# Performance work log

Measured on AMD Instinct MI355X. Metric: run time of the kernel, lower is better.

Reference implementation:

```python
import jax, jax.numpy as jnp
import numpy as np

EPS = 1e-5

def setup_inputs() -> dict:
    key = jax.random.key(0)
    k1, k2 = jax.random.split(key)
    x = jax.random.normal(k1, (16, 512, 128, 128), dtype=jnp.float32)
    classifier_w = jax.random.normal(k2, (19, 512), dtype=jnp.float32)
    sel = jnp.arange(16, dtype=jnp.int32)  # selected_classes
    return {"x": x, "classifier_w": classifier_w, "sel": sel}


def reference(x, classifier_w, sel):
    # x: [B, ch, H, W]; classifier_w: [num_classes, ch]; sel: [C] class ids
    B, ch, H, W = x.shape
    C = sel.shape[0]
    G = ch // C            # number of channel groups
    HW = H * W

    w_abs = jnp.abs(classifier_w)          # [K, ch]
    idx = jnp.argsort(-w_abs, axis=1)      # descending sort indices [K, ch]
    sig = jax.nn.sigmoid(w_abs)            # [K, ch]

    idx_sel = idx[sel]                     # [C, ch]
    ch_ids = idx_sel[:, :G].T              # [G, C]; ch_ids[k, j] = idx[sel[j]][k]
    perm = ch_ids.reshape(G * C)           # output channel C*k+j <- input channel
    wgh = sig[sel[None, :], ch_ids].reshape(G * C)  # sigmoid weights per output channel

    # fused gather + scale (replaces the triple Python loop)
    xs = x[:, perm] * wgh[None, :, None, None]      # [B, G*C, H, W]
    xg = xs.reshape(B, G, C, HW)                    # groups of C channels

    # per-group covariance: bmm(x, x^T) / (HW - 1) + eps*I
    cov = jnp.einsum('bgch,bgdh->bgcd', xg, xg) / (HW - 1)
    cov = cov + EPS * jnp.eye(C, dtype=x.dtype)

    mask = jnp.triu(jnp.ones((C, C), dtype=x.dtype), k=1)  # reversal_i
    num_off = jnp.sum(mask)                # C*(C-1)/2 off-diagonal entries

    # relax_denom == 0 -> margin = 0
    off = jnp.sum(jnp.abs(cov * mask), axis=(2, 3))         # [B, G]
    loss_per = jnp.maximum(off / num_off, 0.0)              # clamp(min=0)
    loss = jnp.sum(loss_per) / B           # per-group mean over B, summed over groups
    return loss.reshape(1)
```

## Files before the change

### kernel.cpp

```cpp
#include <hip/hip_runtime.h>
#include <math.h>

constexpr int B_  = 16;
constexpr int CH  = 512;
constexpr int HW  = 128 * 128;
constexpr int C_  = 16;
constexpr int G_  = 32;
constexpr int NP  = (C_ * (C_ - 1)) / 2;

__global__ __launch_bounds__(64)
void topk_kernel(const float* __restrict__ w, const int* __restrict__ sel,
                 int* __restrict__ perm_tbl, float* __restrict__ wgh_tbl) {
  const int j    = blockIdx.x;
  const int lane = threadIdx.x;
  const float* wr = w + (size_t)sel[j] * CH;

  float vals[8];
#pragma unroll
  for (int i = 0; i < 8; ++i) vals[i] = fabsf(wr[lane * 8 + i]);

  for (int k = 0; k < G_; ++k) {
    float bv = vals[0];
    int bloc = 0;
#pragma unroll
    for (int i = 1; i < 8; ++i)
      if (vals[i] > bv) { bv = vals[i]; bloc = i; }
    int bi = lane * 8 + bloc;

#pragma unroll
    for (int m = 1; m < 64; m <<= 1) {
      float ov = __shfl_xor(bv, m);
      int   oi = __shfl_xor(bi, m);
      if (ov > bv || (ov == bv && oi < bi)) { bv = ov; bi = oi; }
    }

    if (lane == 0) {
      perm_tbl[k * C_ + j] = bi;
      wgh_tbl [k * C_ + j] = 1.0f / (1.0f + expf(-bv));
    }

    if ((bi >> 3) == lane) {
#pragma unroll
      for (int i = 0; i < 8; ++i)
        if ((bi & 7) == i) vals[i] = -1.0f;
    }
  }
}

__global__ __launch_bounds__(256, 2)
void gram_kernel(const float* __restrict__ x, const int* __restrict__ perm_tbl,
                 const float* __restrict__ wgh_tbl, float* __restrict__ out) {
  const int bg = blockIdx.x;
  const int b  = bg >> 5;
  const int g  = bg & (G_ - 1);
  const int t  = threadIdx.x;

  __shared__ int   s_ch[C_];
  __shared__ float s_w[C_];
  if (t < C_) {
    s_ch[t] = perm_tbl[g * C_ + t];
    s_w[t]  = wgh_tbl[g * C_ + t];
  }
  __syncthreads();

  const float* bb = x + (size_t)b * ((size_t)CH * HW);
  int off[C_];
#pragma unroll
  for (int c = 0; c < C_; ++c) off[c] = s_ch[c] * HW;

  float acc[NP];
#pragma unroll
  for (int i = 0; i < NP; ++i) acc[i] = 0.0f;

  for (int it = 0; it < HW / (256 * 2); ++it) {
    const int h = (it * 256 + t) * 2;
    float2 v[C_];
#pragma unroll
    for (int c = 0; c < C_; ++c)
      v[c] = *(const float2*)(bb + off[c] + h);

    int p = 0;
#pragma unroll
    for (int c = 0; c < C_; ++c) {
#pragma unroll
      for (int d = c + 1; d < C_; ++d) {
        acc[p] = fmaf(v[c].x, v[d].x, acc[p]);
        acc[p] = fmaf(v[c].y, v[d].y, acc[p]);
        ++p;
      }
    }
  }

  const int lane = t & 63;
  const int wv   = t >> 6;
#pragma unroll
  for (int i = 0; i < NP; ++i) {
    float a = acc[i];
#pragma unroll
    for (int m = 1; m < 64; m <<= 1) a += __shfl_xor(a, m);
    acc[i] = a;
  }

  __shared__ float s_part[4][NP];
  if (lane == 0) {
#pragma unroll
    for (int i = 0; i < NP; ++i) s_part[wv][i] = acc[i];
  }
  __syncthreads();

  __shared__ float s_fin[128];
  if (t < 128) {
    float s = 0.0f;
    if (t < NP) {
      s = s_part[0][t] + s_part[1][t] + s_part[2][t] + s_part[3][t];
      int cc = 0, rem = t;
      while (rem >= (C_ - 1) - cc) { rem -= (C_ - 1) - cc; ++cc; }
      int dd = cc + 1 + rem;
      s = fabsf(s) * s_w[cc] * s_w[dd];
    }
    s_fin[t] = s;
  }
  __syncthreads();

  for (int st = 64; st > 0; st >>= 1) {
    if (t < st) s_fin[t] += s_fin[t + st];
    __syncthreads();
  }

  if (t == 0) {
    constexpr float SCALE = 1.0f / (120.0f * 16383.0f * 16.0f);
    atomicAdd(out, s_fin[0] * SCALE);
  }
}

extern "C" void kernel_launch(void* const* d_in, const int* in_sizes, int n_in,
                              void* d_out, int out_size, void* d_ws, size_t ws_size,
                              hipStream_t stream) {
  const float* x   = (const float*)d_in[0];
  const float* w   = (const float*)d_in[1];
  const int*   sel = (const int*)d_in[2];
  float*       out = (float*)d_out;

  int*   perm_tbl = (int*)d_ws;
  float* wgh_tbl  = (float*)((char*)d_ws + CH * sizeof(int));

  hipMemsetAsync(d_out, 0, sizeof(float), stream);

  hipLaunchKernelGGL(topk_kernel, dim3(C_), dim3(64), 0, stream,
                     w, sel, perm_tbl, wgh_tbl);
  hipLaunchKernelGGL(gram_kernel, dim3(B_ * G_), dim3(256), 0, stream,
                     x, perm_tbl, wgh_tbl, out);
}
```

Baseline: 687.6 us.

## Split Gram reduction over spatial chunks with a separate finalize kernel

The spatial dimension is split into four chunks, so the Gram kernel launches four times as many blocks. Each block writes partial pair sums to workspace, and a new finalize kernel combines them, applies abs and the sigmoid weights, and does the atomic add. With only 512 blocks on a large GPU the original grid left compute units underused for a bandwidth-bound read of 512MB. The change adds a third kernel launch and a small round trip of partial sums through global memory.

```diff
diff --git a/kernel.cpp b/kernel.cpp
--- a/kernel.cpp
+++ b/kernel.cpp
@@ -7,6 +7,8 @@
 constexpr int C_  = 16;
 constexpr int G_  = 32;
 constexpr int NP  = (C_ * (C_ - 1)) / 2;
+constexpr int NSPLIT = 4;
+constexpr int HWS = HW / NSPLIT;
 
 __global__ __launch_bounds__(64)
 void topk_kernel(const float* __restrict__ w, const int* __restrict__ sel,
@@ -48,22 +50,21 @@
 }
 
 __global__ __launch_bounds__(256, 2)
-void gram_kernel(const float* __restrict__ x, const int* __restrict__ perm_tbl,
-                 const float* __restrict__ wgh_tbl, float* __restrict__ out) {
-  const int bg = blockIdx.x;
-  const int b  = bg >> 5;
-  const int g  = bg & (G_ - 1);
-  const int t  = threadIdx.x;
+void gram_part_kernel(const float* __restrict__ x,
+                      const int* __restrict__ perm_tbl,
+                      float* __restrict__ part) {
+  const int bid   = blockIdx.x;
+  const int split = bid & (NSPLIT - 1);
+  const int bg    = bid >> 2;
+  const int b     = bg >> 5;
+  const int g     = bg & (G_ - 1);
+  const int t     = threadIdx.x;
 
-  __shared__ int   s_ch[C_];
-  __shared__ float s_w[C_];
-  if (t < C_) {
-    s_ch[t] = perm_tbl[g * C_ + t];
-    s_w[t]  = wgh_tbl[g * C_ + t];
-  }
+  __shared__ int s_ch[C_];
+  if (t < C_) s_ch[t] = perm_tbl[g * C_ + t];
   __syncthreads();
 
-  const float* bb = x + (size_t)b * ((size_t)CH * HW);
+  const float* bb = x + (size_t)b * ((size_t)CH * HW) + split * HWS;
   int off[C_];
 #pragma unroll
   for (int c = 0; c < C_; ++c) off[c] = s_ch[c] * HW;
@@ -72,7 +73,7 @@
 #pragma unroll
   for (int i = 0; i < NP; ++i) acc[i] = 0.0f;
 
-  for (int it = 0; it < HW / (256 * 2); ++it) {
+  for (int it = 0; it < HWS / (256 * 2); ++it) {
     const int h = (it * 256 + t) * 2;
     float2 v[C_];
 #pragma unroll
@@ -108,28 +109,41 @@
   }
   __syncthreads();
 
-  __shared__ float s_fin[128];
-  if (t < 128) {
-    float s = 0.0f;
-    if (t < NP) {
-      s = s_part[0][t] + s_part[1][t] + s_part[2][t] + s_part[3][t];
-      int cc = 0, rem = t;
-      while (rem >= (C_ - 1) - cc) { rem -= (C_ - 1) - cc; ++cc; }
-      int dd = cc + 1 + rem;
-      s = fabsf(s) * s_w[cc] * s_w[dd];
-    }
-    s_fin[t] = s;
+  if (t < NP) {
+    part[(size_t)bid * NP + t] =
+        s_part[0][t] + s_part[1][t] + s_part[2][t] + s_part[3][t];
   }
+}
+
+__global__ __launch_bounds__(128)
+void finalize_kernel(const float* __restrict__ part,
+                     const float* __restrict__ wgh_tbl,
+                     float* __restrict__ out) {
+  const int bg = blockIdx.x;
+  const int g  = bg & (G_ - 1);
+  const int t  = threadIdx.x;
+
+  float v = 0.0f;
+  if (t < NP) {
+    const float* p = part + (size_t)bg * NSPLIT * NP + t;
+    float s = p[0] + p[NP] + p[2 * NP] + p[3 * NP];
+    int cc = 0, rem = t;
+    while (rem >= (C_ - 1) - cc) { rem -= (C_ - 1) - cc; ++cc; }
+    int dd = cc + 1 + rem;
+    v = fabsf(s) * wgh_tbl[g * C_ + cc] * wgh_tbl[g * C_ + dd];
+  }
+
+  __shared__ float s_red[128];
+  s_red[t] = v;
   __syncthreads();
-
   for (int st = 64; st > 0; st >>= 1) {
-    if (t < st) s_fin[t] += s_fin[t + st];
+    if (t < st) s_red[t] += s_red[t + st];
     __syncthreads();
   }
 
   if (t == 0) {
     constexpr float SCALE = 1.0f / (120.0f * 16383.0f * 16.0f);
-    atomicAdd(out, s_fin[0] * SCALE);
+    atomicAdd(out, s_red[0] * SCALE);
   }
 }
 
@@ -143,11 +157,14 @@
 
   int*   perm_tbl = (int*)d_ws;
   float* wgh_tbl  = (float*)((char*)d_ws + CH * sizeof(int));
+  float* part     = (float*)((char*)d_ws + 2 * CH * sizeof(int));
 
   hipMemsetAsync(d_out, 0, sizeof(float), stream);
 
   hipLaunchKernelGGL(topk_kernel, dim3(C_), dim3(64), 0, stream,
                      w, sel, perm_tbl, wgh_tbl);
-  hipLaunchKernelGGL(gram_kernel, dim3(B_ * G_), dim3(256), 0, stream,
-                     x, perm_tbl, wgh_tbl, out);
+  hipLaunchKernelGGL(gram_part_kernel, dim3(B_ * G_ * NSPLIT), dim3(256), 0, stream,
+                     x, perm_tbl, part);
+  hipLaunchKernelGGL(finalize_kernel, dim3(B_ * G_), dim3(128), 0, stream,
+                     part, wgh_tbl, out);
 }
```

Measured after the change: 696.3 us. No clear change (+1.3%).
